# Performance work log

Hardware: AMD Instinct MI355X
Metric: run time of the kernel (lower is better)

The kernel has to match this reference:

```python
import jax, jax.numpy as jnp
import numpy as np

N_NODES = 50000
N_GRAPHS = 100
NODES_PER_GRAPH = 500
N_EDGES = 800000
EMB = 128
N_LAYERS = 4
Z_DIM = 2 * EMB + 1  # [x_i, x_j, dist]
BN_EPS = 1e-5


def setup_inputs() -> dict:
    key = jax.random.key(0)
    ks = jax.random.split(key, 12)
    z = jax.random.randint(ks[0], (N_NODES,), 0, 100)
    pos = jax.random.normal(ks[1], (N_NODES, 3), dtype=jnp.float32) * 3.0
    batch = jnp.repeat(jnp.arange(N_GRAPHS), NODES_PER_GRAPH)
    # within-graph random edges (stands in for radius_graph's bounded-degree output)
    rng = np.random.default_rng(0)
    eg = np.repeat(np.arange(N_GRAPHS), N_EDGES // N_GRAPHS)
    src = eg * NODES_PER_GRAPH + rng.integers(0, NODES_PER_GRAPH, N_EDGES)
    dst = eg * NODES_PER_GRAPH + rng.integers(0, NODES_PER_GRAPH, N_EDGES)
    edge_index = jnp.asarray(np.stack([src, dst]), dtype=jnp.int64)
    s = 0.05
    emb = jax.random.normal(ks[2], (100, EMB), dtype=jnp.float32)
    Wf = jax.random.normal(ks[3], (N_LAYERS, Z_DIM, EMB), dtype=jnp.float32) * s
    bf = jnp.zeros((N_LAYERS, EMB), dtype=jnp.float32)
    Ws = jax.random.normal(ks[4], (N_LAYERS, Z_DIM, EMB), dtype=jnp.float32) * s
    bs = jnp.zeros((N_LAYERS, EMB), dtype=jnp.float32)
    bn1_g = jnp.ones((N_LAYERS, EMB), dtype=jnp.float32)
    bn1_b = jnp.zeros((N_LAYERS, EMB), dtype=jnp.float32)
    bn2_g = jnp.ones((N_LAYERS, EMB), dtype=jnp.float32)
    bn2_b = jnp.zeros((N_LAYERS, EMB), dtype=jnp.float32)
    W1 = jax.random.normal(ks[5], (EMB, EMB), dtype=jnp.float32) * s
    b1 = jnp.zeros((EMB,), dtype=jnp.float32)
    W2 = jax.random.normal(ks[6], (EMB, 1), dtype=jnp.float32) * s
    b2 = jnp.zeros((1,), dtype=jnp.float32)
    return {"pos": pos, "emb": emb, "Wf": Wf, "bf": bf, "Ws": Ws, "bs": bs,
            "bn1_g": bn1_g, "bn1_b": bn1_b, "bn2_g": bn2_g, "bn2_b": bn2_b,
            "W1": W1, "b1": b1, "W2": W2, "b2": b2,
            "z": z, "batch": batch, "edge_index": edge_index}


def _batchnorm(x, g, b):
    mu = jnp.mean(x, axis=0)
    var = jnp.var(x, axis=0)  # biased, matches torch BN training normalization
    return (x - mu) * jax.lax.rsqrt(var + BN_EPS) * g + b


def reference(pos, emb, Wf, bf, Ws, bs, bn1_g, bn1_b, bn2_g, bn2_b, W1, b1, W2, b2, z, batch, edge_index):
    j, i = edge_index[0], edge_index[1]  # source j -> target i (PyG flow)
    x = emb[z]  # [N, EMB]
    dist = jnp.linalg.norm(pos[i] - pos[j], axis=-1, keepdims=True)  # [E, 1]
    for l in range(N_LAYERS):
        zc = jnp.concatenate([x[i], x[j], dist], axis=-1)  # [E, 257]
        msg = jax.nn.sigmoid(zc @ Wf[l] + bf[l]) * jax.nn.softplus(zc @ Ws[l] + bs[l])
        agg = jax.ops.segment_sum(msg, i, num_segments=N_NODES)  # CGConv 'add' aggregation
        out = _batchnorm(agg, bn1_g[l], bn1_b[l]) + x  # CGConv internal BN + residual
        x = jax.nn.relu(_batchnorm(out, bn2_g[l], bn2_b[l]))  # outer BN + ReLU (dropout=0)
    # global mean pool over graphs
    gsum = jax.ops.segment_sum(x, batch, num_segments=N_GRAPHS)
    cnt = jax.ops.segment_sum(jnp.ones((N_NODES, 1), x.dtype), batch, num_segments=N_GRAPHS)
    g = gsum / cnt
    h = jax.nn.relu(g @ W1 + b1)
    return (h @ W2 + b2).reshape(-1)  # [N_GRAPHS]
```

## Files before the change

### kernel.cpp

```cpp
#include <hip/hip_runtime.h>

#define NN 50000
#define NG 100
#define NPG 500
#define NE 800000
#define EPG 8000
#define EMBD 128
#define NL 4
#define CS_BLOCKS 1000
#define CS_ROWS 50

typedef __attribute__((ext_vector_type(8))) short short8v;
typedef __attribute__((ext_vector_type(4))) float float4v;
typedef __attribute__((ext_vector_type(2))) float f2;

__device__ __forceinline__ unsigned short f2bf(float v) {
  unsigned u = __float_as_uint(v);
  u += 0x7FFFu + ((u >> 16) & 1u);
  return (unsigned short)(u >> 16);
}
__device__ __forceinline__ float bf2f(unsigned short h) {
  return __uint_as_float(((unsigned)h) << 16);
}

__device__ __forceinline__ float fexp2(float x) {
#if __has_builtin(__builtin_amdgcn_exp2f)
  return __builtin_amdgcn_exp2f(x);
#else
  float r; asm("v_exp_f32 %0, %1" : "=v"(r) : "v"(x)); return r;
#endif
}
__device__ __forceinline__ float flog2(float x) {
#if __has_builtin(__builtin_amdgcn_logf)
  return __builtin_amdgcn_logf(x);
#else
  float r; asm("v_log_f32 %0, %1" : "=v"(r) : "v"(x)); return r;
#endif
}
__device__ __forceinline__ float frcp(float x) {
#if __has_builtin(__builtin_amdgcn_rcpf)
  return __builtin_amdgcn_rcpf(x);
#else
  float r; asm("v_rcp_f32 %0, %1" : "=v"(r) : "v"(x)); return r;
#endif
}

__device__ __forceinline__ f2 unpk(unsigned v) {
  f2 r;
  r.x = __uint_as_float(v << 16);
  r.y = __uint_as_float(v & 0xffff0000u);
  return r;
}

__global__ void prep_w(const float* __restrict__ Wf, const float* __restrict__ Ws,
                       unsigned short* __restrict__ whT) {
  int idx = blockIdx.x * 256 + threadIdx.x;
  int k = idx & 127;
  int oc = (idx >> 7) & 511;
  int l = idx >> 16;
  const float* W;
  int row, c;
  if (oc < 128) { W = Wf; row = k; c = oc; }
  else if (oc < 256) { W = Ws; row = k; c = oc - 128; }
  else {
    int t = oc - 256;
    int p = t >> 2, r = t & 3;
    c = 2 * p + (r & 1);
    W = (r < 2) ? Wf : Ws;
    row = 128 + k;
  }
  whT[idx] = f2bf(W[(size_t)l * 32896 + (size_t)row * 128 + c]);
}

__global__ void gather_x(const float* __restrict__ emb, const int* __restrict__ z,
                         unsigned short* __restrict__ xh) {
  const int total = NN * 32;
  for (int idx = blockIdx.x * 256 + threadIdx.x; idx < total; idx += gridDim.x * 256) {
    int n = idx >> 5, c4 = (idx & 31) * 4;
    float4 v = *(const float4*)(emb + (size_t)z[n] * EMBD + c4);
    ushort4 h;
    h.x = f2bf(v.x); h.y = f2bf(v.y); h.z = f2bf(v.z); h.w = f2bf(v.w);
    *(ushort4*)(xh + (size_t)idx * 4) = h;
  }
}

__global__ __launch_bounds__(512) void csr_build(const int* __restrict__ ei,
                                                 const float* __restrict__ pos,
                                                 int* __restrict__ offs, int* __restrict__ deg,
                                                 uint2* __restrict__ csr) {
  __shared__ int hist[NPG];
  __shared__ int scan[512];
  const int g = blockIdx.x, t = threadIdx.x;
  const int nbase = g * NPG;
  const int e0 = g * EPG;
  for (int n = t; n < NPG; n += 512) hist[n] = 0;
  __syncthreads();
  for (int e = t; e < EPG; e += 512) atomicAdd(&hist[ei[NE + e0 + e] - nbase], 1);
  __syncthreads();
  int v = (t < NPG) ? hist[t] : 0;
  scan[t] = v;
  __syncthreads();
  for (int d = 1; d < 512; d <<= 1) {
    int a = (t >= d) ? scan[t - d] : 0;
    __syncthreads();
    scan[t] += a;
    __syncthreads();
  }
  if (t < NPG) {
    int off = scan[t] - v;
    offs[nbase + t] = e0 + off;
    deg[nbase + t] = v;
    hist[t] = off;
  }
  __syncthreads();
  for (int e = t; e < EPG; e += 512) {
    int j = ei[e0 + e];
    int i = ei[NE + e0 + e];
    float dx = pos[i * 3 + 0] - pos[j * 3 + 0];
    float dy = pos[i * 3 + 1] - pos[j * 3 + 1];
    float dz = pos[i * 3 + 2] - pos[j * 3 + 2];
    float dist = sqrtf(dx * dx + dy * dy + dz * dz);
    int p = atomicAdd(&hist[i - nbase], 1);
    csr[e0 + p] = make_uint2((unsigned)j, __float_as_uint(dist));
  }
}

#define BM 128
#define BN 128
__global__ __launch_bounds__(256, 2) void gemm_proj(const unsigned short* __restrict__ xh,
                                                    const unsigned short* __restrict__ whT,
                                                    unsigned short* __restrict__ P, int l) {
  __shared__ __align__(16) unsigned short smem[32768];
  unsigned short* sA = smem;
  unsigned short* sB = smem + 16384;
  const int tid = threadIdx.x;
  const int R0 = blockIdx.y * BM;
  const int C0 = blockIdx.x * BN;
  for (int gid = tid; gid < BM * 16; gid += 256) {
    int row = gid >> 4, gc = gid & 15;
    int grow = R0 + row;
    uint4 v = make_uint4(0u, 0u, 0u, 0u);
    if (grow < NN) v = *(const uint4*)(xh + (size_t)grow * 128 + gc * 8);
    int gs = (gc & 8) | ((gc ^ row) & 7);
    *(uint4*)((char*)sA + row * 256 + gs * 16) = v;
  }
  for (int gid = tid; gid < BN * 16; gid += 256) {
    int c = gid >> 4, gc = gid & 15;
    uint4 v = *(const uint4*)(whT + ((size_t)l * 512 + C0 + c) * 128 + gc * 8);
    int gs = (gc & 8) | ((gc ^ c) & 7);
    *(uint4*)((char*)sB + c * 256 + gs * 16) = v;
  }
  __syncthreads();
  const int w = tid >> 6, lane = tid & 63;
  const int lr = lane & 15, lk = lane >> 4;
  float4v acc[2][8];
#pragma unroll
  for (int i = 0; i < 2; i++)
#pragma unroll
    for (int j = 0; j < 8; j++) acc[i][j] = (float4v){0.f, 0.f, 0.f, 0.f};
#pragma unroll
  for (int kb = 0; kb < 4; kb++) {
    int g = kb * 4 + lk;
    short8v a[2], b[8];
#pragma unroll
    for (int rf = 0; rf < 2; rf++) {
      int row = w * 32 + rf * 16 + lr;
      int gs = (g & 8) | ((g ^ row) & 7);
      a[rf] = *(const short8v*)((const char*)sA + row * 256 + gs * 16);
    }
#pragma unroll
    for (int cf = 0; cf < 8; cf++) {
      int c = cf * 16 + lr;
      int gs = (g & 8) | ((g ^ c) & 7);
      b[cf] = *(const short8v*)((const char*)sB + c * 256 + gs * 16);
    }
#pragma unroll
    for (int rf = 0; rf < 2; rf++)
#pragma unroll
      for (int cf = 0; cf < 8; cf++)
        acc[rf][cf] = __builtin_amdgcn_mfma_f32_16x16x32_bf16(a[rf], b[cf], acc[rf][cf], 0, 0, 0);
  }
  __syncthreads();
  unsigned short* sC = smem;
#pragma unroll
  for (int rf = 0; rf < 2; rf++) {
#pragma unroll
    for (int cf = 0; cf < 8; cf++) {
      int col = cf * 16 + lr;
#pragma unroll
      for (int j = 0; j < 4; j++) {
        int row = w * 32 + rf * 16 + lk * 4 + j;
        sC[row * 136 + col] = f2bf(acc[rf][cf][j]);
      }
    }
  }
  __syncthreads();
  for (int it = tid; it < BM * 16; it += 256) {
    int row = it >> 4, gc = it & 15;
    int grow = R0 + row;
    if (grow < NN) {
      uint4 v = *(const uint4*)(sC + row * 136 + gc * 8);
      *(uint4*)(P + (size_t)grow * 512 + C0 + gc * 8) = v;
    }
  }
}

__global__ __launch_bounds__(256) void edge_gather(const unsigned short* __restrict__ P,
                                                   const uint2* __restrict__ csr,
                                                   const int* __restrict__ offs,
                                                   const int* __restrict__ deg,
                                                   const float* __restrict__ Wf,
                                                   const float* __restrict__ bf,
                                                   const float* __restrict__ Ws,
                                                   const float* __restrict__ bs,
                                                   unsigned short* __restrict__ aggh, int l) {
  const float L = 1.4426950408889634f;
  const float LN2 = 0.6931471805599453f;
  const int lane = threadIdx.x & 63;
  const int wid = __builtin_amdgcn_readfirstlane(threadIdx.x >> 6);
  const int bid = blockIdx.x;
  const int xcd = bid & 7, bidx = bid >> 3;
  const int wg = (xcd < 4) ? xcd * 1563 + bidx : 4 * 1563 + (xcd - 4) * 1562 + bidx;
  const int i = wg * 4 + wid;
  const int f0 = lane * 2;

  const unsigned* Piu = (const unsigned*)(P + (size_t)i * 512);
  unsigned pif = Piu[lane];
  unsigned pis = Piu[64 + lane];

  float2 wfd = *(const float2*)(Wf + (size_t)l * 32896 + 256 * 128 + f0);
  float2 wsd = *(const float2*)(Ws + (size_t)l * 32896 + 256 * 128 + f0);
  float2 bfv = *(const float2*)(bf + l * 128 + f0);
  float2 bsv = *(const float2*)(bs + l * 128 + f0);

  f2 bflv, bslv, wflv, wslv;
  {
    f2 pi_f = unpk(pif), pi_s = unpk(pis);
    bflv.x = (pi_f.x + bfv.x) * L; bflv.y = (pi_f.y + bfv.y) * L;
    bslv.x = (pi_s.x + bsv.x) * L; bslv.y = (pi_s.y + bsv.y) * L;
    wflv.x = wfd.x * L; wflv.y = wfd.y * L;
    wslv.x = wsd.x * L; wslv.y = wsd.y * L;
  }

  const int off = __builtin_amdgcn_readfirstlane(offs[i]);
  const int nd = __builtin_amdgcn_readfirstlane(deg[i]);
  const uint2* ep = csr + off;
  f2 acc = (f2){0.f, 0.f};

#define EDGE_BODY(DVU, V)                                          \
  {                                                                \
    float dv = __uint_as_float(DVU);                               \
    f2 pf = unpk((V).x) * L + (bflv + dv * wflv);                  \
    f2 ps = unpk((V).y) * L + (bslv + dv * wslv);                  \
    f2 a, b, r, lg;                                                \
    a.x = fexp2(-pf.x); a.y = fexp2(-pf.y);                        \
    b.x = fexp2(ps.x);  b.y = fexp2(ps.y);                         \
    r.x = frcp(a.x + 1.f); r.y = frcp(a.y + 1.f);                  \
    lg.x = flog2(b.x + 1.f); lg.y = flog2(b.y + 1.f);              \
    acc += r * lg;                                                 \
  }

  int k = 0;
  for (; k + 3 < nd; k += 4) {
    uint2 e0 = ep[k], e1 = ep[k + 1], e2 = ep[k + 2], e3 = ep[k + 3];
    unsigned j0 = __builtin_amdgcn_readfirstlane(e0.x);
    unsigned j1 = __builtin_amdgcn_readfirstlane(e1.x);
    unsigned j2 = __builtin_amdgcn_readfirstlane(e2.x);
    unsigned j3 = __builtin_amdgcn_readfirstlane(e3.x);
    unsigned d0 = __builtin_amdgcn_readfirstlane(e0.y);
    unsigned d1 = __builtin_amdgcn_readfirstlane(e1.y);
    unsigned d2 = __builtin_amdgcn_readfirstlane(e2.y);
    unsigned d3 = __builtin_amdgcn_readfirstlane(e3.y);
    uint2 v0 = ((const uint2*)(P + (size_t)j0 * 512))[64 + lane];
    uint2 v1 = ((const uint2*)(P + (size_t)j1 * 512))[64 + lane];
    uint2 v2 = ((const uint2*)(P + (size_t)j2 * 512))[64 + lane];
    uint2 v3 = ((const uint2*)(P + (size_t)j3 * 512))[64 + lane];
    EDGE_BODY(d0, v0)
    EDGE_BODY(d1, v1)
    EDGE_BODY(d2, v2)
    EDGE_BODY(d3, v3)
  }
  for (; k < nd; k++) {
    uint2 e0 = ep[k];
    unsigned j0 = __builtin_amdgcn_readfirstlane(e0.x);
    unsigned d0 = __builtin_amdgcn_readfirstlane(e0.y);
    uint2 v0 = ((const uint2*)(P + (size_t)j0 * 512))[64 + lane];
    EDGE_BODY(d0, v0)
  }
#undef EDGE_BODY

  acc.x *= LN2; acc.y *= LN2;
  unsigned packed = ((unsigned)f2bf(acc.y) << 16) | (unsigned)f2bf(acc.x);
  ((unsigned*)(aggh + (size_t)i * EMBD))[lane] = packed;
}

__global__ __launch_bounds__(256) void col_stats(const unsigned short* __restrict__ aggh,
                                                 const unsigned short* __restrict__ xh,
                                                 float* __restrict__ partial) {
  const int b = blockIdx.x, tid = threadIdx.x;
  const int c4 = tid & 31;
  const int h = tid >> 5;
  const int r0 = b * CS_ROWS;
  float4 sa = {0, 0, 0, 0}, sa2 = {0, 0, 0, 0}, sx = {0, 0, 0, 0}, sx2 = {0, 0, 0, 0},
         sax = {0, 0, 0, 0};
  for (int rr = h; rr < CS_ROWS; rr += 8) {
    size_t idx = (size_t)(r0 + rr) * EMBD + c4 * 4;
    ushort4 ha = *(const ushort4*)(aggh + idx);
    ushort4 hx = *(const ushort4*)(xh + idx);
    float a0 = bf2f(ha.x), a1 = bf2f(ha.y), a2 = bf2f(ha.z), a3 = bf2f(ha.w);
    float x0 = bf2f(hx.x), x1 = bf2f(hx.y), x2 = bf2f(hx.z), x3 = bf2f(hx.w);
    sa.x += a0; sa.y += a1; sa.z += a2; sa.w += a3;
    sa2.x += a0 * a0; sa2.y += a1 * a1; sa2.z += a2 * a2; sa2.w += a3 * a3;
    sx.x += x0; sx.y += x1; sx.z += x2; sx.w += x3;
    sx2.x += x0 * x0; sx2.y += x1 * x1; sx2.z += x2 * x2; sx2.w += x3 * x3;
    sax.x += a0 * x0; sax.y += a1 * x1; sax.z += a2 * x2; sax.w += a3 * x3;
  }
  __shared__ float4 sm[256];
  float* p = partial + (size_t)b * 640;
#define REDUCE_STAT(V, OUTOFF)                                              \
  sm[tid] = V;                                                              \
  __syncthreads();                                                          \
  if (h == 0) {                                                             \
    float4 s = sm[tid];                                                     \
    for (int g = 1; g < 8; g++) {                                           \
      float4 o = sm[g * 32 + tid];                                          \
      s.x += o.x; s.y += o.y; s.z += o.z; s.w += o.w;                       \
    }                                                                       \
    *(float4*)(p + (OUTOFF) + c4 * 4) = s;                                  \
  }                                                                         \
  __syncthreads();
  REDUCE_STAT(sa, 0)
  REDUCE_STAT(sa2, 128)
  REDUCE_STAT(sx, 256)
  REDUCE_STAT(sx2, 384)
  REDUCE_STAT(sax, 512)
#undef REDUCE_STAT
}

__global__ __launch_bounds__(256) void bn_fold(const float* __restrict__ partial,
                                               const float* __restrict__ bn1g,
                                               const float* __restrict__ bn1b,
                                               const float* __restrict__ bn2g,
                                               const float* __restrict__ bn2b,
                                               float* __restrict__ abc, int l) {
  __shared__ float sm[5 * 256];
  const int t = threadIdx.x;
  const int ci = t & 15;
  const int col = blockIdx.x * 16 + ci;
  const int chunk = t >> 4;
  float s0 = 0, s1 = 0, s2 = 0, s3 = 0, s4 = 0;
  for (int b = chunk; b < CS_BLOCKS; b += 16) {
    const float* p = partial + (size_t)b * 640 + col;
    s0 += p[0]; s1 += p[128]; s2 += p[256]; s3 += p[384]; s4 += p[512];
  }
  sm[t] = s0; sm[256 + t] = s1; sm[512 + t] = s2; sm[768 + t] = s3; sm[1024 + t] = s4;
  __syncthreads();
  if (t < 16) {
    int c = blockIdx.x * 16 + t;
    float a0 = 0, a1 = 0, a2 = 0, a3 = 0, a4 = 0;
    for (int ch = 0; ch < 16; ch++) {
      int u = ch * 16 + t;
      a0 += sm[u]; a1 += sm[256 + u]; a2 += sm[512 + u]; a3 += sm[768 + u]; a4 += sm[1024 + u];
    }
    const double Ninv = 1.0 / (double)NN;
    double Ea = a0 * Ninv, Ea2 = a1 * Ninv, Ex = a2 * Ninv, Ex2 = a3 * Ninv, Eax = a4 * Ninv;
    double var1 = Ea2 - Ea * Ea;
    double g1 = bn1g[l * 128 + c], b1 = bn1b[l * 128 + c];
    double g2 = bn2g[l * 128 + c], b2v = bn2b[l * 128 + c];
    double s1d = g1 / sqrt(var1 + 1e-5);
    double t1 = b1 - Ea * s1d;
    double mu_o = s1d * Ea + t1 + Ex;
    double Eo2 = s1d * s1d * Ea2 + 2.0 * s1d * t1 * Ea + t1 * t1 + 2.0 * (s1d * Eax + t1 * Ex) + Ex2;
    double var_o = Eo2 - mu_o * mu_o;
    double s2d = g2 / sqrt(var_o + 1e-5);
    double t2 = b2v - mu_o * s2d;
    abc[c] = (float)(s1d * s2d);
    abc[128 + c] = (float)s2d;
    abc[256 + c] = (float)(t1 * s2d + t2);
  }
}

__global__ void fuse_bn(const unsigned short* __restrict__ aggh, unsigned short* __restrict__ xh,
                        const float* __restrict__ abc) {
  const int total = NN * 32;
  for (int idx = blockIdx.x * 256 + threadIdx.x; idx < total; idx += gridDim.x * 256) {
    int c4 = (idx & 31) * 4;
    size_t base = (size_t)idx * 4;
    ushort4 ha = *(const ushort4*)(aggh + base);
    ushort4 hx = *(const ushort4*)(xh + base);
    float4 A = *(const float4*)(abc + c4);
    float4 B = *(const float4*)(abc + 128 + c4);
    float4 C = *(const float4*)(abc + 256 + c4);
    float4 o;
    o.x = fmaxf(fmaf(A.x, bf2f(ha.x), fmaf(B.x, bf2f(hx.x), C.x)), 0.f);
    o.y = fmaxf(fmaf(A.y, bf2f(ha.y), fmaf(B.y, bf2f(hx.y), C.y)), 0.f);
    o.z = fmaxf(fmaf(A.z, bf2f(ha.z), fmaf(B.z, bf2f(hx.z), C.z)), 0.f);
    o.w = fmaxf(fmaf(A.w, bf2f(ha.w), fmaf(B.w, bf2f(hx.w), C.w)), 0.f);
    ushort4 hh;
    hh.x = f2bf(o.x); hh.y = f2bf(o.y); hh.z = f2bf(o.z); hh.w = f2bf(o.w);
    *(ushort4*)(xh + base) = hh;
  }
}

__global__ __launch_bounds__(512) void pool_mlp(const unsigned short* __restrict__ xh,
                                                const float* __restrict__ W1,
                                                const float* __restrict__ b1,
                                                const float* __restrict__ W2,
                                                const float* __restrict__ b2,
                                                float* __restrict__ out) {
  __shared__ float red[512];
  __shared__ float gl[128];
  const int g = blockIdx.x, t = threadIdx.x;
  const int c = t & 127, q = t >> 7;
  const unsigned short* bx = xh + (size_t)g * NPG * EMBD;
  float s = 0.f;
  for (int r = q; r < NPG; r += 4) s += bf2f(bx[(size_t)r * EMBD + c]);
  red[t] = s;
  __syncthreads();
  if (q == 0) gl[c] = (red[c] + red[128 + c] + red[256 + c] + red[384 + c]) * (1.f / NPG);
  __syncthreads();
  float acc = 0.f;
  for (int k = q * 32; k < q * 32 + 32; k++) acc = fmaf(gl[k], W1[k * EMBD + c], acc);
  red[t] = acc;
  __syncthreads();
  if (q == 0) {
    float h = fmaxf(red[c] + red[128 + c] + red[256 + c] + red[384 + c] + b1[c], 0.f);
    red[c] = h * W2[c];
  }
  __syncthreads();
  for (int sft = 64; sft > 0; sft >>= 1) {
    if (t < sft) red[t] += red[t + sft];
    __syncthreads();
  }
  if (t == 0) out[g] = red[0] + b2[0];
}

extern "C" void kernel_launch(void* const* d_in, const int* in_sizes, int n_in,
                              void* d_out, int out_size, void* d_ws, size_t ws_size,
                              hipStream_t stream) {
  const float* pos = (const float*)d_in[0];
  const float* emb = (const float*)d_in[1];
  const float* Wf = (const float*)d_in[2];
  const float* bf = (const float*)d_in[3];
  const float* Ws = (const float*)d_in[4];
  const float* bs = (const float*)d_in[5];
  const float* bn1g = (const float*)d_in[6];
  const float* bn1b = (const float*)d_in[7];
  const float* bn2g = (const float*)d_in[8];
  const float* bn2b = (const float*)d_in[9];
  const float* W1 = (const float*)d_in[10];
  const float* b1 = (const float*)d_in[11];
  const float* W2 = (const float*)d_in[12];
  const float* b2 = (const float*)d_in[13];
  const int* z = (const int*)d_in[14];
  const int* ei = (const int*)d_in[16];
  float* out = (float*)d_out;

  char* ws = (char*)d_ws;
  unsigned short* xh = (unsigned short*)(ws + 0);
  unsigned short* P = (unsigned short*)(ws + 12800000);
  unsigned short* aggh = (unsigned short*)(ws + 64000000);
  uint2* csr = (uint2*)(ws + 76800000);
  int* deg = (int*)(ws + 83200000);
  int* offs = (int*)(ws + 83400000);
  unsigned short* whT = (unsigned short*)(ws + 83600000);
  float* partial = (float*)(ws + 84124288);
  float* abc = (float*)(ws + 86684288);

  prep_w<<<1024, 256, 0, stream>>>(Wf, Ws, whT);
  gather_x<<<2048, 256, 0, stream>>>(emb, z, xh);
  csr_build<<<NG, 512, 0, stream>>>(ei, pos, offs, deg, csr);
  for (int l = 0; l < NL; l++) {
    gemm_proj<<<dim3(4, 391), 256, 0, stream>>>(xh, whT, P, l);
    edge_gather<<<NN / 4, 256, 0, stream>>>(P, csr, offs, deg, Wf, bf, Ws, bs, aggh, l);
    col_stats<<<CS_BLOCKS, 256, 0, stream>>>(aggh, xh, partial);
    bn_fold<<<8, 256, 0, stream>>>(partial, bn1g, bn1b, bn2g, bn2b, abc, l);
    fuse_bn<<<2048, 256, 0, stream>>>(aggh, xh, abc);
  }
  pool_mlp<<<NG, 512, 0, stream>>>(xh, W1, b1, W2, b2, out);
}
```

Measured before the change: 540.0 us.

## Fuse column statistics into edge_gather and fuse_bn, drop col_stats kernel

```diff
diff --git a/kernel.cpp b/kernel.cpp
--- a/kernel.cpp
+++ b/kernel.cpp
@@ -7,8 +7,9 @@
 #define EPG 8000
 #define EMBD 128
 #define NL 4
-#define CS_BLOCKS 1000
-#define CS_ROWS 50
+#define EB_BLOCKS 3125
+#define FB_BLOCKS 1000
+#define FB_ROWS 50
 
 typedef __attribute__((ext_vector_type(8))) short short8v;
 typedef __attribute__((ext_vector_type(4))) float float4v;
@@ -72,16 +73,41 @@
   whT[idx] = f2bf(W[(size_t)l * 32896 + (size_t)row * 128 + c]);
 }
 
-__global__ void gather_x(const float* __restrict__ emb, const int* __restrict__ z,
-                         unsigned short* __restrict__ xh) {
-  const int total = NN * 32;
-  for (int idx = blockIdx.x * 256 + threadIdx.x; idx < total; idx += gridDim.x * 256) {
-    int n = idx >> 5, c4 = (idx & 31) * 4;
-    float4 v = *(const float4*)(emb + (size_t)z[n] * EMBD + c4);
-    ushort4 h;
-    h.x = f2bf(v.x); h.y = f2bf(v.y); h.z = f2bf(v.z); h.w = f2bf(v.w);
-    *(ushort4*)(xh + (size_t)idx * 4) = h;
-  }
+__global__ __launch_bounds__(256) void gather_x(const float* __restrict__ emb,
+                                                const int* __restrict__ z,
+                                                unsigned short* __restrict__ xh,
+                                                float* __restrict__ partial_x) {
+  const int b = blockIdx.x, tid = threadIdx.x;
+  const int c4 = tid & 31, h = tid >> 5;
+  const int r0 = b * FB_ROWS;
+  float4 sx = {0, 0, 0, 0}, sx2 = {0, 0, 0, 0};
+  for (int rr = h; rr < FB_ROWS; rr += 8) {
+    int n = r0 + rr;
+    float4 v = *(const float4*)(emb + (size_t)z[n] * EMBD + c4 * 4);
+    ushort4 hh;
+    hh.x = f2bf(v.x); hh.y = f2bf(v.y); hh.z = f2bf(v.z); hh.w = f2bf(v.w);
+    *(ushort4*)(xh + (size_t)n * EMBD + c4 * 4) = hh;
+    float o0 = bf2f(hh.x), o1 = bf2f(hh.y), o2 = bf2f(hh.z), o3 = bf2f(hh.w);
+    sx.x += o0; sx.y += o1; sx.z += o2; sx.w += o3;
+    sx2.x += o0 * o0; sx2.y += o1 * o1; sx2.z += o2 * o2; sx2.w += o3 * o3;
+  }
+  __shared__ float4 sm[256];
+  float* p = partial_x + (size_t)b * 256;
+#define REDUCE_STAT(V, OUTOFF)                                              \
+  sm[tid] = V;                                                              \
+  __syncthreads();                                                          \
+  if (h == 0) {                                                             \
+    float4 s = sm[tid];                                                     \
+    for (int g = 1; g < 8; g++) {                                           \
+      float4 o = sm[g * 32 + tid];                                          \
+      s.x += o.x; s.y += o.y; s.z += o.z; s.w += o.w;                       \
+    }                                                                       \
+    *(float4*)(p + (OUTOFF) + c4 * 4) = s;                                  \
+  }                                                                         \
+  __syncthreads();
+  REDUCE_STAT(sx, 0)
+  REDUCE_STAT(sx2, 128)
+#undef REDUCE_STAT
 }
 
 __global__ __launch_bounds__(512) void csr_build(const int* __restrict__ ei,
@@ -213,39 +239,27 @@
                                                    const float* __restrict__ bf,
                                                    const float* __restrict__ Ws,
                                                    const float* __restrict__ bs,
-                                                   unsigned short* __restrict__ aggh, int l) {
+                                                   const unsigned short* __restrict__ xh,
+                                                   unsigned short* __restrict__ aggh,
+                                                   float* __restrict__ partial_a, int l) {
   const float L = 1.4426950408889634f;
   const float LN2 = 0.6931471805599453f;
   const int lane = threadIdx.x & 63;
   const int wid = __builtin_amdgcn_readfirstlane(threadIdx.x >> 6);
   const int bid = blockIdx.x;
   const int xcd = bid & 7, bidx = bid >> 3;
-  const int wg = (xcd < 4) ? xcd * 1563 + bidx : 4 * 1563 + (xcd - 4) * 1562 + bidx;
-  const int i = wg * 4 + wid;
+  const int wg = (xcd < 5) ? xcd * 391 + bidx : 5 * 391 + (xcd - 5) * 390 + bidx;
   const int f0 = lane * 2;
-
-  const unsigned* Piu = (const unsigned*)(P + (size_t)i * 512);
-  unsigned pif = Piu[lane];
-  unsigned pis = Piu[64 + lane];
 
   float2 wfd = *(const float2*)(Wf + (size_t)l * 32896 + 256 * 128 + f0);
   float2 wsd = *(const float2*)(Ws + (size_t)l * 32896 + 256 * 128 + f0);
   float2 bfv = *(const float2*)(bf + l * 128 + f0);
   float2 bsv = *(const float2*)(bs + l * 128 + f0);
-
-  f2 bflv, bslv, wflv, wslv;
-  {
-    f2 pi_f = unpk(pif), pi_s = unpk(pis);
-    bflv.x = (pi_f.x + bfv.x) * L; bflv.y = (pi_f.y + bfv.y) * L;
-    bslv.x = (pi_s.x + bsv.x) * L; bslv.y = (pi_s.y + bsv.y) * L;
-    wflv.x = wfd.x * L; wflv.y = wfd.y * L;
-    wslv.x = wsd.x * L; wslv.y = wsd.y * L;
-  }
-
-  const int off = __builtin_amdgcn_readfirstlane(offs[i]);
-  const int nd = __builtin_amdgcn_readfirstlane(deg[i]);
-  const uint2* ep = csr + off;
-  f2 acc = (f2){0.f, 0.f};
+  f2 wflv, wslv;
+  wflv.x = wfd.x * L; wflv.y = wfd.y * L;
+  wslv.x = wsd.x * L; wslv.y = wsd.y * L;
+
+  f2 sa = (f2){0.f, 0.f}, sa2 = (f2){0.f, 0.f}, sax = (f2){0.f, 0.f};
 
 #define EDGE_BODY(DVU, V)                                          \
   {                                                                \
@@ -260,84 +274,82 @@
     acc += r * lg;                                                 \
   }
 
-  int k = 0;
-  for (; k + 3 < nd; k += 4) {
-    uint2 e0 = ep[k], e1 = ep[k + 1], e2 = ep[k + 2], e3 = ep[k + 3];
-    unsigned j0 = __builtin_amdgcn_readfirstlane(e0.x);
-    unsigned j1 = __builtin_amdgcn_readfirstlane(e1.x);
-    unsigned j2 = __builtin_amdgcn_readfirstlane(e2.x);
-    unsigned j3 = __builtin_amdgcn_readfirstlane(e3.x);
-    unsigned d0 = __builtin_amdgcn_readfirstlane(e0.y);
-    unsigned d1 = __builtin_amdgcn_readfirstlane(e1.y);
-    unsigned d2 = __builtin_amdgcn_readfirstlane(e2.y);
-    unsigned d3 = __builtin_amdgcn_readfirstlane(e3.y);
-    uint2 v0 = ((const uint2*)(P + (size_t)j0 * 512))[64 + lane];
-    uint2 v1 = ((const uint2*)(P + (size_t)j1 * 512))[64 + lane];
-    uint2 v2 = ((const uint2*)(P + (size_t)j2 * 512))[64 + lane];
-    uint2 v3 = ((const uint2*)(P + (size_t)j3 * 512))[64 + lane];
-    EDGE_BODY(d0, v0)
-    EDGE_BODY(d1, v1)
-    EDGE_BODY(d2, v2)
-    EDGE_BODY(d3, v3)
-  }
-  for (; k < nd; k++) {
-    uint2 e0 = ep[k];
-    unsigned j0 = __builtin_amdgcn_readfirstlane(e0.x);
-    unsigned d0 = __builtin_amdgcn_readfirstlane(e0.y);
-    uint2 v0 = ((const uint2*)(P + (size_t)j0 * 512))[64 + lane];
-    EDGE_BODY(d0, v0)
+  for (int n = 0; n < 4; n++) {
+    const int i = wg * 16 + wid * 4 + n;
+    const unsigned* Piu = (const unsigned*)(P + (size_t)i * 512);
+    unsigned pif = Piu[lane];
+    unsigned pis = Piu[64 + lane];
+    f2 bflv, bslv;
+    {
+      f2 pi_f = unpk(pif), pi_s = unpk(pis);
+      bflv.x = (pi_f.x + bfv.x) * L; bflv.y = (pi_f.y + bfv.y) * L;
+      bslv.x = (pi_s.x + bsv.x) * L; bslv.y = (pi_s.y + bsv.y) * L;
+    }
+    const int off = __builtin_amdgcn_readfirstlane(offs[i]);
+    const int nd = __builtin_amdgcn_readfirstlane(deg[i]);
+    const uint2* ep = csr + off;
+    f2 acc = (f2){0.f, 0.f};
+    int k = 0;
+    for (; k + 3 < nd; k += 4) {
+      uint2 e0 = ep[k], e1 = ep[k + 1], e2 = ep[k + 2], e3 = ep[k + 3];
+      unsigned j0 = __builtin_amdgcn_readfirstlane(e0.x);
+      unsigned j1 = __builtin_amdgcn_readfirstlane(e1.x);
+      unsigned j2 = __builtin_amdgcn_readfirstlane(e2.x);
+      unsigned j3 = __builtin_amdgcn_readfirstlane(e3.x);
+      unsigned d0 = __builtin_amdgcn_readfirstlane(e0.y);
+      unsigned d1 = __builtin_amdgcn_readfirstlane(e1.y);
+      unsigned d2 = __builtin_amdgcn_readfirstlane(e2.y);
+      unsigned d3 = __builtin_amdgcn_readfirstlane(e3.y);
+      uint2 v0 = ((const uint2*)(P + (size_t)j0 * 512))[64 + lane];
+      uint2 v1 = ((const uint2*)(P + (size_t)j1 * 512))[64 + lane];
+      uint2 v2 = ((const uint2*)(P + (size_t)j2 * 512))[64 + lane];
+      uint2 v3 = ((const uint2*)(P + (size_t)j3 * 512))[64 + lane];
+      EDGE_BODY(d0, v0)
+      EDGE_BODY(d1, v1)
+      EDGE_BODY(d2, v2)
+      EDGE_BODY(d3, v3)
+    }
+    for (; k < nd; k++) {
+      uint2 e0 = ep[k];
+      unsigned j0 = __builtin_amdgcn_readfirstlane(e0.x);
+      unsigned d0 = __builtin_amdgcn_readfirstlane(e0.y);
+      uint2 v0 = ((const uint2*)(P + (size_t)j0 * 512))[64 + lane];
+      EDGE_BODY(d0, v0)
+    }
+    acc.x *= LN2; acc.y *= LN2;
+    unsigned packed = ((unsigned)f2bf(acc.y) << 16) | (unsigned)f2bf(acc.x);
+    ((unsigned*)(aggh + (size_t)i * EMBD))[lane] = packed;
+    f2 aggr = unpk(packed);
+    f2 xv = unpk(((const unsigned*)(xh + (size_t)i * EMBD))[lane]);
+    sa += aggr;
+    sa2 += aggr * aggr;
+    sax += aggr * xv;
   }
 #undef EDGE_BODY
 
-  acc.x *= LN2; acc.y *= LN2;
-  unsigned packed = ((unsigned)f2bf(acc.y) << 16) | (unsigned)f2bf(acc.x);
-  ((unsigned*)(aggh + (size_t)i * EMBD))[lane] = packed;
-}
-
-__global__ __launch_bounds__(256) void col_stats(const unsigned short* __restrict__ aggh,
-                                                 const unsigned short* __restrict__ xh,
-                                                 float* __restrict__ partial) {
-  const int b = blockIdx.x, tid = threadIdx.x;
-  const int c4 = tid & 31;
-  const int h = tid >> 5;
-  const int r0 = b * CS_ROWS;
-  float4 sa = {0, 0, 0, 0}, sa2 = {0, 0, 0, 0}, sx = {0, 0, 0, 0}, sx2 = {0, 0, 0, 0},
-         sax = {0, 0, 0, 0};
-  for (int rr = h; rr < CS_ROWS; rr += 8) {
-    size_t idx = (size_t)(r0 + rr) * EMBD + c4 * 4;
-    ushort4 ha = *(const ushort4*)(aggh + idx);
-    ushort4 hx = *(const ushort4*)(xh + idx);
-    float a0 = bf2f(ha.x), a1 = bf2f(ha.y), a2 = bf2f(ha.z), a3 = bf2f(ha.w);
-    float x0 = bf2f(hx.x), x1 = bf2f(hx.y), x2 = bf2f(hx.z), x3 = bf2f(hx.w);
-    sa.x += a0; sa.y += a1; sa.z += a2; sa.w += a3;
-    sa2.x += a0 * a0; sa2.y += a1 * a1; sa2.z += a2 * a2; sa2.w += a3 * a3;
-    sx.x += x0; sx.y += x1; sx.z += x2; sx.w += x3;
-    sx2.x += x0 * x0; sx2.y += x1 * x1; sx2.z += x2 * x2; sx2.w += x3 * x3;
-    sax.x += a0 * x0; sax.y += a1 * x1; sax.z += a2 * x2; sax.w += a3 * x3;
-  }
-  __shared__ float4 sm[256];
-  float* p = partial + (size_t)b * 640;
-#define REDUCE_STAT(V, OUTOFF)                                              \
-  sm[tid] = V;                                                              \
-  __syncthreads();                                                          \
-  if (h == 0) {                                                             \
-    float4 s = sm[tid];                                                     \
-    for (int g = 1; g < 8; g++) {                                           \
-      float4 o = sm[g * 32 + tid];                                          \
-      s.x += o.x; s.y += o.y; s.z += o.z; s.w += o.w;                       \
-    }                                                                       \
-    *(float4*)(p + (OUTOFF) + c4 * 4) = s;                                  \
-  }                                                                         \
-  __syncthreads();
-  REDUCE_STAT(sa, 0)
-  REDUCE_STAT(sa2, 128)
-  REDUCE_STAT(sx, 256)
-  REDUCE_STAT(sx2, 384)
-  REDUCE_STAT(sax, 512)
-#undef REDUCE_STAT
-}
-
-__global__ __launch_bounds__(256) void bn_fold(const float* __restrict__ partial,
+  __shared__ float sm[4 * 64 * 6];
+  int base = (wid * 64 + lane) * 6;
+  sm[base + 0] = sa.x; sm[base + 1] = sa.y;
+  sm[base + 2] = sa2.x; sm[base + 3] = sa2.y;
+  sm[base + 4] = sax.x; sm[base + 5] = sax.y;
+  __syncthreads();
+  if (wid == 0) {
+    f2 ta = sa, ta2 = sa2, tax = sax;
+    for (int w2 = 1; w2 < 4; w2++) {
+      int b2 = (w2 * 64 + lane) * 6;
+      ta.x += sm[b2 + 0]; ta.y += sm[b2 + 1];
+      ta2.x += sm[b2 + 2]; ta2.y += sm[b2 + 3];
+      tax.x += sm[b2 + 4]; tax.y += sm[b2 + 5];
+    }
+    float* p = partial_a + (size_t)bid * 384;
+    *(float2*)(p + f0) = make_float2(ta.x, ta.y);
+    *(float2*)(p + 128 + f0) = make_float2(ta2.x, ta2.y);
+    *(float2*)(p + 256 + f0) = make_float2(tax.x, tax.y);
+  }
+}
+
+__global__ __launch_bounds__(256) void bn_fold(const float* __restrict__ partial_a,
+                                               const float* __restrict__ partial_x,
                                                const float* __restrict__ bn1g,
                                                const float* __restrict__ bn1b,
                                                const float* __restrict__ bn2g,
@@ -345,25 +357,29 @@
                                                float* __restrict__ abc, int l) {
   __shared__ float sm[5 * 256];
   const int t = threadIdx.x;
-  const int ci = t & 15;
-  const int col = blockIdx.x * 16 + ci;
-  const int chunk = t >> 4;
+  const int ci = t & 7;
+  const int col = blockIdx.x * 8 + ci;
+  const int chunk = t >> 3;
   float s0 = 0, s1 = 0, s2 = 0, s3 = 0, s4 = 0;
-  for (int b = chunk; b < CS_BLOCKS; b += 16) {
-    const float* p = partial + (size_t)b * 640 + col;
-    s0 += p[0]; s1 += p[128]; s2 += p[256]; s3 += p[384]; s4 += p[512];
+  for (int b = chunk; b < EB_BLOCKS; b += 32) {
+    const float* p = partial_a + (size_t)b * 384 + col;
+    s0 += p[0]; s1 += p[128]; s2 += p[256];
+  }
+  for (int b = chunk; b < FB_BLOCKS; b += 32) {
+    const float* p = partial_x + (size_t)b * 256 + col;
+    s3 += p[0]; s4 += p[128];
   }
   sm[t] = s0; sm[256 + t] = s1; sm[512 + t] = s2; sm[768 + t] = s3; sm[1024 + t] = s4;
   __syncthreads();
-  if (t < 16) {
-    int c = blockIdx.x * 16 + t;
+  if (t < 8) {
+    int c = blockIdx.x * 8 + t;
     float a0 = 0, a1 = 0, a2 = 0, a3 = 0, a4 = 0;
-    for (int ch = 0; ch < 16; ch++) {
-      int u = ch * 16 + t;
+    for (int ch = 0; ch < 32; ch++) {
+      int u = ch * 8 + t;
       a0 += sm[u]; a1 += sm[256 + u]; a2 += sm[512 + u]; a3 += sm[768 + u]; a4 += sm[1024 + u];
     }
     const double Ninv = 1.0 / (double)NN;
-    double Ea = a0 * Ninv, Ea2 = a1 * Ninv, Ex = a2 * Ninv, Ex2 = a3 * Ninv, Eax = a4 * Ninv;
+    double Ea = a0 * Ninv, Ea2 = a1 * Ninv, Eax = a2 * Ninv, Ex = a3 * Ninv, Ex2 = a4 * Ninv;
     double var1 = Ea2 - Ea * Ea;
     double g1 = bn1g[l * 128 + c], b1 = bn1b[l * 128 + c];
     double g2 = bn2g[l * 128 + c], b2v = bn2b[l * 128 + c];
@@ -380,17 +396,21 @@
   }
 }
 
-__global__ void fuse_bn(const unsigned short* __restrict__ aggh, unsigned short* __restrict__ xh,
-                        const float* __restrict__ abc) {
-  const int total = NN * 32;
-  for (int idx = blockIdx.x * 256 + threadIdx.x; idx < total; idx += gridDim.x * 256) {
-    int c4 = (idx & 31) * 4;
-    size_t base = (size_t)idx * 4;
+__global__ __launch_bounds__(256) void fuse_bn(const unsigned short* __restrict__ aggh,
+                                               unsigned short* __restrict__ xh,
+                                               const float* __restrict__ abc,
+                                               float* __restrict__ partial_x) {
+  const int b = blockIdx.x, tid = threadIdx.x;
+  const int c4 = tid & 31, h = tid >> 5;
+  const int r0 = b * FB_ROWS;
+  float4 A = *(const float4*)(abc + c4 * 4);
+  float4 B = *(const float4*)(abc + 128 + c4 * 4);
+  float4 C = *(const float4*)(abc + 256 + c4 * 4);
+  float4 sx = {0, 0, 0, 0}, sx2 = {0, 0, 0, 0};
+  for (int rr = h; rr < FB_ROWS; rr += 8) {
+    size_t base = (size_t)(r0 + rr) * EMBD + c4 * 4;
     ushort4 ha = *(const ushort4*)(aggh + base);
     ushort4 hx = *(const ushort4*)(xh + base);
-    float4 A = *(const float4*)(abc + c4);
-    float4 B = *(const float4*)(abc + 128 + c4);
-    float4 C = *(const float4*)(abc + 256 + c4);
     float4 o;
     o.x = fmaxf(fmaf(A.x, bf2f(ha.x), fmaf(B.x, bf2f(hx.x), C.x)), 0.f);
     o.y = fmaxf(fmaf(A.y, bf2f(ha.y), fmaf(B.y, bf2f(hx.y), C.y)), 0.f);
@@ -399,7 +419,27 @@
     ushort4 hh;
     hh.x = f2bf(o.x); hh.y = f2bf(o.y); hh.z = f2bf(o.z); hh.w = f2bf(o.w);
     *(ushort4*)(xh + base) = hh;
-  }
+    float o0 = bf2f(hh.x), o1 = bf2f(hh.y), o2 = bf2f(hh.z), o3 = bf2f(hh.w);
+    sx.x += o0; sx.y += o1; sx.z += o2; sx.w += o3;
+    sx2.x += o0 * o0; sx2.y += o1 * o1; sx2.z += o2 * o2; sx2.w += o3 * o3;
+  }
+  __shared__ float4 sm[256];
+  float* p = partial_x + (size_t)b * 256;
+#define REDUCE_STAT(V, OUTOFF)                                              \
+  sm[tid] = V;                                                              \
+  __syncthreads();                                                          \
+  if (h == 0) {                                                             \
+    float4 s = sm[tid];                                                     \
+    for (int g = 1; g < 8; g++) {                                           \
+      float4 o = sm[g * 32 + tid];                                          \
+      s.x += o.x; s.y += o.y; s.z += o.z; s.w += o.w;                       \
+    }                                                                       \
+    *(float4*)(p + (OUTOFF) + c4 * 4) = s;                                  \
+  }                                                                         \
+  __syncthreads();
+  REDUCE_STAT(sx, 0)
+  REDUCE_STAT(sx2, 128)
+#undef REDUCE_STAT
 }
 
 __global__ __launch_bounds__(512) void pool_mlp(const unsigned short* __restrict__ xh,
@@ -464,18 +504,19 @@
   int* deg = (int*)(ws + 83200000);
   int* offs = (int*)(ws + 83400000);
   unsigned short* whT = (unsigned short*)(ws + 83600000);
-  float* partial = (float*)(ws + 84124288);
-  float* abc = (float*)(ws + 86684288);
+  float* partial_a = (float*)(ws + 84124288);
+  float* partial_x = (float*)(ws + 88924288);
+  float* abc = (float*)(ws + 89948288);
 
   prep_w<<<1024, 256, 0, stream>>>(Wf, Ws, whT);
-  gather_x<<<2048, 256, 0, stream>>>(emb, z, xh);
+  gather_x<<<FB_BLOCKS, 256, 0, stream>>>(emb, z, xh, partial_x);
   csr_build<<<NG, 512, 0, stream>>>(ei, pos, offs, deg, csr);
   for (int l = 0; l < NL; l++) {
     gemm_proj<<<dim3(4, 391), 256, 0, stream>>>(xh, whT, P, l);
-    edge_gather<<<NN / 4, 256, 0, stream>>>(P, csr, offs, deg, Wf, bf, Ws, bs, aggh, l);
-    col_stats<<<CS_BLOCKS, 256, 0, stream>>>(aggh, xh, partial);
-    bn_fold<<<8, 256, 0, stream>>>(partial, bn1g, bn1b, bn2g, bn2b, abc, l);
-    fuse_bn<<<2048, 256, 0, stream>>>(aggh, xh, abc);
+    edge_gather<<<EB_BLOCKS, 256, 0, stream>>>(P, csr, offs, deg, Wf, bf, Ws, bs, xh, aggh,
+                                               partial_a, l);
+    bn_fold<<<16, 256, 0, stream>>>(partial_a, partial_x, bn1g, bn1b, bn2g, bn2b, abc, l);
+    fuse_bn<<<FB_BLOCKS, 256, 0, stream>>>(aggh, xh, abc, partial_x);
   }
   pool_mlp<<<NG, 512, 0, stream>>>(xh, W1, b1, W2, b2, out);
 }
```

Result: slower. 618.8 us (+14.6%).

## Fuse BN-apply and ReLU into next GEMM prologue and pooling kernel

Applied to the files above, without the earlier changes.

```diff
diff --git a/kernel.cpp b/kernel.cpp
--- a/kernel.cpp
+++ b/kernel.cpp
@@ -127,20 +127,47 @@
 
 #define BM 128
 #define BN 128
-__global__ __launch_bounds__(256, 2) void gemm_proj(const unsigned short* __restrict__ xh,
+__global__ __launch_bounds__(256, 2) void gemm_proj(const unsigned short* __restrict__ xh_old,
+                                                    const unsigned short* __restrict__ aggh,
+                                                    const float* __restrict__ abc,
                                                     const unsigned short* __restrict__ whT,
-                                                    unsigned short* __restrict__ P, int l) {
+                                                    unsigned short* __restrict__ P,
+                                                    unsigned short* __restrict__ xh_new, int l) {
   __shared__ __align__(16) unsigned short smem[32768];
+  __shared__ float sABC[384];
   unsigned short* sA = smem;
   unsigned short* sB = smem + 16384;
   const int tid = threadIdx.x;
   const int R0 = blockIdx.y * BM;
   const int C0 = blockIdx.x * BN;
+  if (l > 0) {
+    for (int t = tid; t < 384; t += 256) sABC[t] = abc[t];
+  }
+  __syncthreads();
   for (int gid = tid; gid < BM * 16; gid += 256) {
     int row = gid >> 4, gc = gid & 15;
     int grow = R0 + row;
     uint4 v = make_uint4(0u, 0u, 0u, 0u);
-    if (grow < NN) v = *(const uint4*)(xh + (size_t)grow * 128 + gc * 8);
+    if (grow < NN) {
+      if (l == 0) {
+        v = *(const uint4*)(xh_old + (size_t)grow * 128 + gc * 8);
+      } else {
+        uint4 va = *(const uint4*)(aggh + (size_t)grow * 128 + gc * 8);
+        uint4 vx = *(const uint4*)(xh_old + (size_t)grow * 128 + gc * 8);
+        const unsigned* pa = (const unsigned*)&va;
+        const unsigned* px = (const unsigned*)&vx;
+        unsigned* pv = (unsigned*)&v;
+#pragma unroll
+        for (int q = 0; q < 4; q++) {
+          f2 ag = unpk(pa[q]), xv = unpk(px[q]);
+          int c0 = gc * 8 + q * 2;
+          float o0 = fmaxf(fmaf(sABC[c0], ag.x, fmaf(sABC[128 + c0], xv.x, sABC[256 + c0])), 0.f);
+          float o1 = fmaxf(fmaf(sABC[c0 + 1], ag.y, fmaf(sABC[129 + c0], xv.y, sABC[257 + c0])), 0.f);
+          pv[q] = ((unsigned)f2bf(o1) << 16) | (unsigned)f2bf(o0);
+        }
+        if (C0 == 0) *(uint4*)(xh_new + (size_t)grow * 128 + gc * 8) = v;
+      }
+    }
     int gs = (gc & 8) | ((gc ^ row) & 7);
     *(uint4*)((char*)sA + row * 256 + gs * 16) = v;
   }
@@ -380,29 +407,9 @@
   }
 }
 
-__global__ void fuse_bn(const unsigned short* __restrict__ aggh, unsigned short* __restrict__ xh,
-                        const float* __restrict__ abc) {
-  const int total = NN * 32;
-  for (int idx = blockIdx.x * 256 + threadIdx.x; idx < total; idx += gridDim.x * 256) {
-    int c4 = (idx & 31) * 4;
-    size_t base = (size_t)idx * 4;
-    ushort4 ha = *(const ushort4*)(aggh + base);
-    ushort4 hx = *(const ushort4*)(xh + base);
-    float4 A = *(const float4*)(abc + c4);
-    float4 B = *(const float4*)(abc + 128 + c4);
-    float4 C = *(const float4*)(abc + 256 + c4);
-    float4 o;
-    o.x = fmaxf(fmaf(A.x, bf2f(ha.x), fmaf(B.x, bf2f(hx.x), C.x)), 0.f);
-    o.y = fmaxf(fmaf(A.y, bf2f(ha.y), fmaf(B.y, bf2f(hx.y), C.y)), 0.f);
-    o.z = fmaxf(fmaf(A.z, bf2f(ha.z), fmaf(B.z, bf2f(hx.z), C.z)), 0.f);
-    o.w = fmaxf(fmaf(A.w, bf2f(ha.w), fmaf(B.w, bf2f(hx.w), C.w)), 0.f);
-    ushort4 hh;
-    hh.x = f2bf(o.x); hh.y = f2bf(o.y); hh.z = f2bf(o.z); hh.w = f2bf(o.w);
-    *(ushort4*)(xh + base) = hh;
-  }
-}
-
-__global__ __launch_bounds__(512) void pool_mlp(const unsigned short* __restrict__ xh,
+__global__ __launch_bounds__(512) void pool_mlp(const unsigned short* __restrict__ aggh,
+                                                const unsigned short* __restrict__ xh,
+                                                const float* __restrict__ abc,
                                                 const float* __restrict__ W1,
                                                 const float* __restrict__ b1,
                                                 const float* __restrict__ W2,
@@ -410,11 +417,19 @@
                                                 float* __restrict__ out) {
   __shared__ float red[512];
   __shared__ float gl[128];
+  __shared__ float sABC[384];
   const int g = blockIdx.x, t = threadIdx.x;
+  for (int u = t; u < 384; u += 512) sABC[u] = abc[u];
+  __syncthreads();
   const int c = t & 127, q = t >> 7;
+  const float A = sABC[c], B = sABC[128 + c], C = sABC[256 + c];
+  const unsigned short* bagg = aggh + (size_t)g * NPG * EMBD;
   const unsigned short* bx = xh + (size_t)g * NPG * EMBD;
   float s = 0.f;
-  for (int r = q; r < NPG; r += 4) s += bf2f(bx[(size_t)r * EMBD + c]);
+  for (int r = q; r < NPG; r += 4) {
+    size_t idx = (size_t)r * EMBD + c;
+    s += fmaxf(fmaf(A, bf2f(bagg[idx]), fmaf(B, bf2f(bx[idx]), C)), 0.f);
+  }
   red[t] = s;
   __syncthreads();
   if (q == 0) gl[c] = (red[c] + red[128 + c] + red[256 + c] + red[384 + c]) * (1.f / NPG);
@@ -457,25 +472,29 @@
   float* out = (float*)d_out;
 
   char* ws = (char*)d_ws;
-  unsigned short* xh = (unsigned short*)(ws + 0);
-  unsigned short* P = (unsigned short*)(ws + 12800000);
-  unsigned short* aggh = (unsigned short*)(ws + 64000000);
-  uint2* csr = (uint2*)(ws + 76800000);
-  int* deg = (int*)(ws + 83200000);
-  int* offs = (int*)(ws + 83400000);
-  unsigned short* whT = (unsigned short*)(ws + 83600000);
-  float* partial = (float*)(ws + 84124288);
-  float* abc = (float*)(ws + 86684288);
+  unsigned short* xhA = (unsigned short*)(ws + 0);
+  unsigned short* xhB = (unsigned short*)(ws + 12800000);
+  unsigned short* P = (unsigned short*)(ws + 25600000);
+  unsigned short* aggh = (unsigned short*)(ws + 76800000);
+  uint2* csr = (uint2*)(ws + 89600000);
+  int* deg = (int*)(ws + 96000000);
+  int* offs = (int*)(ws + 96200000);
+  unsigned short* whT = (unsigned short*)(ws + 96400000);
+  float* partial = (float*)(ws + 96924288);
+  float* abc = (float*)(ws + 99484288);
+
+  unsigned short* xb[2] = {xhA, xhB};
+  int cur = 0;
 
   prep_w<<<1024, 256, 0, stream>>>(Wf, Ws, whT);
-  gather_x<<<2048, 256, 0, stream>>>(emb, z, xh);
+  gather_x<<<2048, 256, 0, stream>>>(emb, z, xhA);
   csr_build<<<NG, 512, 0, stream>>>(ei, pos, offs, deg, csr);
   for (int l = 0; l < NL; l++) {
-    gemm_proj<<<dim3(4, 391), 256, 0, stream>>>(xh, whT, P, l);
+    gemm_proj<<<dim3(4, 391), 256, 0, stream>>>(xb[cur], aggh, abc, whT, P, xb[cur ^ 1], l);
+    if (l > 0) cur ^= 1;
     edge_gather<<<NN / 4, 256, 0, stream>>>(P, csr, offs, deg, Wf, bf, Ws, bs, aggh, l);
-    col_stats<<<CS_BLOCKS, 256, 0, stream>>>(aggh, xh, partial);
+    col_stats<<<CS_BLOCKS, 256, 0, stream>>>(aggh, xb[cur], partial);
     bn_fold<<<8, 256, 0, stream>>>(partial, bn1g, bn1b, bn2g, bn2b, abc, l);
-    fuse_bn<<<2048, 256, 0, stream>>>(aggh, xh, abc);
-  }
-  pool_mlp<<<NG, 512, 0, stream>>>(xh, W1, b1, W2, b2, out);
-}
+  }
+  pool_mlp<<<NG, 512, 0, stream>>>(aggh, xb[cur], abc, W1, b1, W2, b2, out);
+}
```

After: 551.9 us. +2.2%, slower.
